# Optimization experiments

Measured on AMD Instinct MI355X. Metric: run time of the kernel, lower is better.

## Reference

```python
import jax, jax.numpy as jnp
import numpy as np

DIM, HEADS, DHEAD, CTX_DIM = 1024, 16, 64, 768
INNER = HEADS * DHEAD  # 1024
FF_HID = 4 * DIM       # 4096
EPS = 1e-5


def _ln(x, g, b):
    mu = jnp.mean(x, axis=-1, keepdims=True)
    var = jnp.mean(jnp.square(x - mu), axis=-1, keepdims=True)
    return (x - mu) * jax.lax.rsqrt(var + EPS) * g + b


def _attn(x, ctx, Wq, Wk, Wv, Wo, bo):
    b, n, _ = x.shape
    m = ctx.shape[1]
    q = (x @ Wq).reshape(b, n, HEADS, DHEAD)
    k = (ctx @ Wk).reshape(b, m, HEADS, DHEAD)
    v = (ctx @ Wv).reshape(b, m, HEADS, DHEAD)
    scale = DHEAD ** -0.5
    sim = jnp.einsum('bihd,bjhd->bhij', q, k) * scale
    attn = jax.nn.softmax(sim, axis=-1)
    out = jnp.einsum('bhij,bjhd->bihd', attn, v).reshape(b, n, INNER)
    return out @ Wo + bo


def setup_inputs() -> dict:
    key = jax.random.key(0)
    ks = jax.random.split(key, 24)
    def w(k, shape, fan_in):
        return jax.random.normal(k, shape, jnp.float32) * (fan_in ** -0.5)
    inp = {
        'x': jax.random.normal(ks[0], (2, 2048, DIM), jnp.float32),
        'context': jax.random.normal(ks[1], (2, 77, CTX_DIM), jnp.float32),
        # attn1 (self)
        'Wq1': w(ks[2], (DIM, INNER), DIM), 'Wk1': w(ks[3], (DIM, INNER), DIM),
        'Wv1': w(ks[4], (DIM, INNER), DIM), 'Wo1': w(ks[5], (INNER, DIM), INNER),
        'bo1': jnp.zeros((DIM,), jnp.float32),
        # attn2 (cross)
        'Wq2': w(ks[6], (DIM, INNER), DIM), 'Wk2': w(ks[7], (CTX_DIM, INNER), CTX_DIM),
        'Wv2': w(ks[8], (CTX_DIM, INNER), CTX_DIM), 'Wo2': w(ks[9], (INNER, DIM), INNER),
        'bo2': jnp.zeros((DIM,), jnp.float32),
        # GEGLU FFN
        'Wp': w(ks[10], (DIM, 2 * FF_HID), DIM), 'bp': jnp.zeros((2 * FF_HID,), jnp.float32),
        'W2': w(ks[11], (FF_HID, DIM), FF_HID), 'b2': jnp.zeros((DIM,), jnp.float32),
        # LayerNorms
        'g1': jnp.ones((DIM,), jnp.float32), 'be1': jnp.zeros((DIM,), jnp.float32),
        'g2': jnp.ones((DIM,), jnp.float32), 'be2': jnp.zeros((DIM,), jnp.float32),
        'g3': jnp.ones((DIM,), jnp.float32), 'be3': jnp.zeros((DIM,), jnp.float32),
    }
    return inp


def reference(x, context, Wq1, Wk1, Wv1, Wo1, bo1, Wq2, Wk2, Wv2, Wo2, bo2,
              Wp, bp, W2, b2, g1, be1, g2, be2, g3, be3):
    h = _ln(x, g1, be1)
    x = _attn(h, h, Wq1, Wk1, Wv1, Wo1, bo1) + x
    h = _ln(x, g2, be2)
    x = _attn(h, context, Wq2, Wk2, Wv2, Wo2, bo2) + x
    h = _ln(x, g3, be3)
    y = h @ Wp + bp
    a, gate = y[..., :FF_HID], y[..., FF_HID:]
    x = (a * jax.nn.gelu(gate, approximate=False)) @ W2 + b2 + x
    return x
```

## Files before the change

kernel.cpp:

```cpp
#include <hip/hip_runtime.h>
#include <hip/hip_bf16.h>
#include <math.h>

#define DIMN   1024
#define HEADS  16
#define DHEAD  64
#define CTXD   768
#define FFH    4096
#define NTOK   4096
#define SEQ    2048
#define NCTX   77
#define CTOK   154

typedef unsigned short u16;
typedef __bf16 bf16x8 __attribute__((ext_vector_type(8)));
typedef float  f32x4  __attribute__((ext_vector_type(4)));

__device__ __forceinline__ u16 f2bf(float f) {
  union { float f; unsigned u; } c; c.f = f;
  unsigned r = c.u + 0x7FFFu + ((c.u >> 16) & 1u);
  return (u16)(r >> 16);
}
__device__ __forceinline__ float bf2f(u16 h) {
  union { unsigned u; float f; } c; c.u = ((unsigned)h) << 16; return c.f;
}

__device__ __forceinline__ void gload16(const void* g, void* l) {
  __builtin_amdgcn_global_load_lds(
      (__attribute__((address_space(1))) void*)(void*)(g),
      (__attribute__((address_space(3))) void*)(l), 16, 0, 0);
}

__device__ __forceinline__ f32x4 mfma16(bf16x8 a, bf16x8 b, f32x4 c) {
  return __builtin_amdgcn_mfma_f32_16x16x32_bf16(a, b, c, 0, 0, 0);
}

struct WAll {
  int nw;
  int start[10];
  const float* s[10];
  u16* d[10];
  int K[10];
  int N[10];
};

__global__ __launch_bounds__(256)
void wconvA_k(WAll wa)
{
  __shared__ u16 t[64][65];
  const int bid = blockIdx.x;
  int w = 0;
  while (w + 1 < wa.nw && bid >= wa.start[w + 1]) ++w;
  const int local = bid - wa.start[w];
  const float* __restrict__ W  = wa.s[w];
  u16* __restrict__       WT   = wa.d[w];
  const int K = wa.K[w], N = wa.N[w];
  const int tilesX = N >> 6;
  const int n0 = (local % tilesX) * 64;
  const int k0 = (local / tilesX) * 64;
  const int tid = threadIdx.x;
  const int rr = tid >> 4, cc = tid & 15;
#pragma unroll
  for (int i = 0; i < 4; ++i) {
    int kr = rr + i * 16;
    const float4 v = *(const float4*)&W[(size_t)(k0 + kr) * N + n0 + cc * 4];
    t[kr][cc*4+0] = f2bf(v.x); t[kr][cc*4+1] = f2bf(v.y);
    t[kr][cc*4+2] = f2bf(v.z); t[kr][cc*4+3] = f2bf(v.w);
  }
  __syncthreads();
#pragma unroll
  for (int i = 0; i < 4; ++i) {
    int nr = rr + i * 16;
    int r0 = cc * 4;
    ushort4 o;
    o.x = t[r0+0][nr]; o.y = t[r0+1][nr]; o.z = t[r0+2][nr]; o.w = t[r0+3][nr];
    *(ushort4*)&WT[(size_t)(n0 + nr) * K + k0 + r0] = o;
  }
}

__global__ void cconv_k(const float* __restrict__ c, u16* __restrict__ o, int n)
{
  int i = blockIdx.x * 256 + threadIdx.x;
  if (i < n) o[i] = f2bf(c[i]);
}

__global__ __launch_bounds__(256)
void ln_k(const float* __restrict__ x, const float* __restrict__ gm,
          const float* __restrict__ bt, u16* __restrict__ o)
{
  int row = blockIdx.x;
  int tid = threadIdx.x;
  const float4 v = *(const float4*)&x[(size_t)row * DIMN + tid * 4];
  float s = v.x + v.y + v.z + v.w;
  float q = v.x*v.x + v.y*v.y + v.z*v.z + v.w*v.w;
#pragma unroll
  for (int off = 32; off; off >>= 1) { s += __shfl_xor(s, off); q += __shfl_xor(q, off); }
  __shared__ float ss[4], qq[4];
  int wave = tid >> 6;
  if ((tid & 63) == 0) { ss[wave] = s; qq[wave] = q; }
  __syncthreads();
  s = ss[0] + ss[1] + ss[2] + ss[3];
  q = qq[0] + qq[1] + qq[2] + qq[3];
  float mu = s * (1.0f / DIMN);
  float var = q * (1.0f / DIMN) - mu * mu;
  float rs = rsqrtf(var + 1e-5f);
  const float4 gv = *(const float4*)&gm[tid * 4];
  const float4 bv = *(const float4*)&bt[tid * 4];
  ushort4 r;
  r.x = f2bf((v.x - mu) * rs * gv.x + bv.x);
  r.y = f2bf((v.y - mu) * rs * gv.y + bv.y);
  r.z = f2bf((v.z - mu) * rs * gv.z + bv.z);
  r.w = f2bf((v.w - mu) * rs * gv.w + bv.w);
  *(ushort4*)&o[(size_t)row * DIMN + tid * 4] = r;
}

__global__ __launch_bounds__(256)
void ln_b_k(const u16* __restrict__ x, const float* __restrict__ gm,
            const float* __restrict__ bt, u16* __restrict__ o)
{
  int row = blockIdx.x;
  int tid = threadIdx.x;
  const ushort4 u = *(const ushort4*)&x[(size_t)row * DIMN + tid * 4];
  float4 v;
  v.x = bf2f(u.x); v.y = bf2f(u.y); v.z = bf2f(u.z); v.w = bf2f(u.w);
  float s = v.x + v.y + v.z + v.w;
  float q = v.x*v.x + v.y*v.y + v.z*v.z + v.w*v.w;
#pragma unroll
  for (int off = 32; off; off >>= 1) { s += __shfl_xor(s, off); q += __shfl_xor(q, off); }
  __shared__ float ss[4], qq[4];
  int wave = tid >> 6;
  if ((tid & 63) == 0) { ss[wave] = s; qq[wave] = q; }
  __syncthreads();
  s = ss[0] + ss[1] + ss[2] + ss[3];
  q = qq[0] + qq[1] + qq[2] + qq[3];
  float mu = s * (1.0f / DIMN);
  float var = q * (1.0f / DIMN) - mu * mu;
  float rs = rsqrtf(var + 1e-5f);
  const float4 gv = *(const float4*)&gm[tid * 4];
  const float4 bv = *(const float4*)&bt[tid * 4];
  ushort4 r;
  r.x = f2bf((v.x - mu) * rs * gv.x + bv.x);
  r.y = f2bf((v.y - mu) * rs * gv.y + bv.y);
  r.z = f2bf((v.z - mu) * rs * gv.z + bv.z);
  r.w = f2bf((v.w - mu) * rs * gv.w + bv.w);
  *(ushort4*)&o[(size_t)row * DIMN + tid * 4] = r;
}

template<int MODE>
__global__ __launch_bounds__(512, 4)
void gemm_k(const u16* __restrict__ A, const u16* __restrict__ Bt,
            int M, int N, int K,
            const float* __restrict__ bias, const float* __restrict__ resid,
            u16* __restrict__ obf, float* __restrict__ of32,
            int seq, int vstride,
            u16* __restrict__ ob2, u16* __restrict__ ob3)
{
  __shared__ __align__(16) u16 As[2][128 * 32];
  __shared__ __align__(16) u16 Bs[2][128 * 32];
  const int tid = threadIdx.x;
  const int lane = tid & 63, wave = tid >> 6;
  const int wr = wave >> 1, wc = wave & 1;
  const int g = lane >> 4, r16 = lane & 15;
  const int m0 = blockIdx.x * 128, n0 = blockIdx.y * 128;

  f32x4 acc[2][4] = {};

  const int srow = tid >> 2;
  const int sch  = tid & 3;
  const int schs = sch ^ ((srow >> 1) & 3);
  const int arow = (m0 + srow > M - 1) ? (M - 1) : (m0 + srow);
  const size_t abase = (size_t)arow * K + schs * 8;
  const size_t bbase = (size_t)(n0 + srow) * K + schs * 8;

  auto stage = [&](int buf, int kt) {
    gload16(A  + abase + kt, &As[buf][tid * 8]);
    gload16(Bt + bbase + kt, &Bs[buf][tid * 8]);
  };

  stage(0, 0);

  const int nkt = K >> 5;
  for (int t = 0; t < nkt; ++t) {
    const int cur = t & 1;
    if (t + 1 < nkt) {
      stage(cur ^ 1, (t + 1) << 5);
      asm volatile("s_waitcnt vmcnt(2)" ::: "memory");
    } else {
      asm volatile("s_waitcnt vmcnt(0)" ::: "memory");
    }
    __builtin_amdgcn_s_barrier();

    bf16x8 af[2], bfr[4];
#pragma unroll
    for (int mi = 0; mi < 2; ++mi) {
      int r = wr * 32 + mi * 16 + r16;
      int cph = g ^ ((r >> 1) & 3);
      af[mi] = *(const bf16x8*)&As[cur][(r * 4 + cph) * 8];
    }
#pragma unroll
    for (int ni = 0; ni < 4; ++ni) {
      int r = wc * 64 + ni * 16 + r16;
      int cph = g ^ ((r >> 1) & 3);
      bfr[ni] = *(const bf16x8*)&Bs[cur][(r * 4 + cph) * 8];
    }
    __builtin_amdgcn_s_setprio(1);
#pragma unroll
    for (int mi = 0; mi < 2; ++mi)
#pragma unroll
      for (int ni = 0; ni < 4; ++ni)
        acc[mi][ni] = mfma16(af[mi], bfr[ni], acc[mi][ni]);
    __builtin_amdgcn_s_setprio(0);

    __builtin_amdgcn_s_barrier();
  }

  const int grp = n0 >> 10;
#pragma unroll
  for (int ni = 0; ni < 4; ++ni) {
    int col = n0 + wc * 64 + ni * 16 + r16;
    const int c1 = col & 1023;
#pragma unroll
    for (int mi = 0; mi < 2; ++mi) {
      f32x4 c = acc[mi][ni];
#pragma unroll
      for (int rg = 0; rg < 4; ++rg) {
        int row = m0 + wr * 32 + mi * 16 + g * 4 + rg;
        if (row < M) {
          float v = c[rg];
          if constexpr (MODE == 4) {
            if (grp == 0) {
              obf[(size_t)row * 1024 + c1] = f2bf(v);
            } else if (grp == 1) {
              ob2[(size_t)row * 1024 + c1] = f2bf(v);
            } else {
              int b = row / seq, srow_ = row - b * seq;
              int jg = srow_ >> 6, j = srow_ & 63;
              int pos = jg * 64 + ((j & 15) << 2) + (j >> 4);
              ob3[((size_t)b * HEADS * DHEAD + c1) * vstride + pos] = f2bf(v);
            }
          }
        }
      }
    }
  }
  (void)bias; (void)resid; (void)of32;
}

template<int MODE>
__global__ __launch_bounds__(512, 2)
void gemm64_k(const u16* __restrict__ A, const u16* __restrict__ Bt,
              int M, int N, int K,
              const float* __restrict__ bias, const float* __restrict__ residf,
              const u16* __restrict__ residb,
              u16* __restrict__ obf, float* __restrict__ of32)
{
  __shared__ __align__(16) u16 As[2][128 * 64];
  __shared__ __align__(16) u16 Bs[2][128 * 64];
  const int tid = threadIdx.x;
  const int lane = tid & 63, wave = tid >> 6;
  const int wr = wave >> 1, wc = wave & 1;
  const int g = lane >> 4, r16 = lane & 15;
  const int m0 = blockIdx.x * 128, n0 = blockIdx.y * 128;

  f32x4 acc[2][4] = {};

  int aro[2], bro[2], scs[2];
#pragma unroll
  for (int i = 0; i < 2; ++i) {
    const int c = tid + i * 512;
    const int r = c >> 3, ch = c & 7;
    scs[i] = ch ^ (r & 7);
    aro[i] = (m0 + r > M - 1) ? (M - 1) : (m0 + r);
    bro[i] = n0 + r;
  }

  auto stage = [&](int buf, int kt) {
#pragma unroll
    for (int i = 0; i < 2; ++i) {
      const int c = tid + i * 512;
      gload16(A  + (size_t)aro[i] * K + kt + scs[i] * 8, &As[buf][c * 8]);
      gload16(Bt + (size_t)bro[i] * K + kt + scs[i] * 8, &Bs[buf][c * 8]);
    }
  };

  stage(0, 0);

  const int nkt = K >> 6;
  for (int t = 0; t < nkt; ++t) {
    const int cur = t & 1;
    if (t + 1 < nkt) {
      stage(cur ^ 1, (t + 1) << 6);
      asm volatile("s_waitcnt vmcnt(4)" ::: "memory");
    } else {
      asm volatile("s_waitcnt vmcnt(0)" ::: "memory");
    }
    __builtin_amdgcn_s_barrier();

#pragma unroll
    for (int ks = 0; ks < 2; ++ks) {
      bf16x8 af[2], bfr[4];
#pragma unroll
      for (int mi = 0; mi < 2; ++mi) {
        int r = wr * 32 + mi * 16 + r16;
        int cph = (ks * 4 + g) ^ (r & 7);
        af[mi] = *(const bf16x8*)&As[cur][(r * 8 + cph) * 8];
      }
#pragma unroll
      for (int ni = 0; ni < 4; ++ni) {
        int r = wc * 64 + ni * 16 + r16;
        int cph = (ks * 4 + g) ^ (r & 7);
        bfr[ni] = *(const bf16x8*)&Bs[cur][(r * 8 + cph) * 8];
      }
      __builtin_amdgcn_s_setprio(1);
#pragma unroll
      for (int mi = 0; mi < 2; ++mi)
#pragma unroll
        for (int ni = 0; ni < 4; ++ni)
          acc[mi][ni] = mfma16(af[mi], bfr[ni], acc[mi][ni]);
      __builtin_amdgcn_s_setprio(0);
    }

    __builtin_amdgcn_s_barrier();
  }

#pragma unroll
  for (int ni = 0; ni < 4; ++ni) {
    int col = n0 + wc * 64 + ni * 16 + r16;
    float bv = bias ? bias[col] : 0.0f;
#pragma unroll
    for (int mi = 0; mi < 2; ++mi) {
      f32x4 c = acc[mi][ni];
#pragma unroll
      for (int rg = 0; rg < 4; ++rg) {
        int row = m0 + wr * 32 + mi * 16 + g * 4 + rg;
        if (row < M) {
          float v = c[rg] + bv;
          size_t o = (size_t)row * N + col;
          if constexpr (MODE == 0) {
            obf[o] = f2bf(v);
          } else if constexpr (MODE == 6) {
            obf[o] = f2bf(v + residf[o]);
          } else if constexpr (MODE == 7) {
            obf[o] = f2bf(v + bf2f(residb[o]));
          } else {
            of32[o] = v + bf2f(residb[o]);
          }
        }
      }
    }
  }
}

__global__ __launch_bounds__(512, 2)
void q2kv2_k(const u16* __restrict__ hb, const u16* __restrict__ WqT2,
             u16* __restrict__ qb,
             const u16* __restrict__ ctxb, const u16* __restrict__ WkT2,
             u16* __restrict__ k2b, u16* __restrict__ vt2b)
{
  __shared__ __align__(16) u16 AsB[2][128 * 64];
  __shared__ __align__(16) u16 BsB[2][128 * 64];
  const int tid = threadIdx.x;
  const int lane = tid & 63, wave = tid >> 6;
  const int wr = wave >> 1, wc = wave & 1;
  const int g = lane >> 4, r16 = lane & 15;
  const int bid = blockIdx.x;

  if (bid < 256) {
    const int K = 1024;
    const int m0 = (bid & 31) * 128, n0 = (bid >> 5) * 128;
    f32x4 acc[2][4] = {};

    int aro[2], bro[2], scs[2];
#pragma unroll
    for (int i = 0; i < 2; ++i) {
      const int c = tid + i * 512;
      const int r = c >> 3, ch = c & 7;
      scs[i] = ch ^ (r & 7);
      aro[i] = m0 + r;
      bro[i] = n0 + r;
    }
    auto stage = [&](int buf, int kt) {
#pragma unroll
      for (int i = 0; i < 2; ++i) {
        const int c = tid + i * 512;
        gload16(hb   + (size_t)aro[i] * K + kt + scs[i] * 8, &AsB[buf][c * 8]);
        gload16(WqT2 + (size_t)bro[i] * K + kt + scs[i] * 8, &BsB[buf][c * 8]);
      }
    };
    stage(0, 0);
    const int nkt = K >> 6;
    for (int t = 0; t < nkt; ++t) {
      const int cur = t & 1;
      if (t + 1 < nkt) {
        stage(cur ^ 1, (t + 1) << 6);
        asm volatile("s_waitcnt vmcnt(4)" ::: "memory");
      } else {
        asm volatile("s_waitcnt vmcnt(0)" ::: "memory");
      }
      __builtin_amdgcn_s_barrier();
#pragma unroll
      for (int ks = 0; ks < 2; ++ks) {
        bf16x8 af[2], bfr[4];
#pragma unroll
        for (int mi = 0; mi < 2; ++mi) {
          int r = wr * 32 + mi * 16 + r16;
          int cph = (ks * 4 + g) ^ (r & 7);
          af[mi] = *(const bf16x8*)&AsB[cur][(r * 8 + cph) * 8];
        }
#pragma unroll
        for (int ni = 0; ni < 4; ++ni) {
          int r = wc * 64 + ni * 16 + r16;
          int cph = (ks * 4 + g) ^ (r & 7);
          bfr[ni] = *(const bf16x8*)&BsB[cur][(r * 8 + cph) * 8];
        }
        __builtin_amdgcn_s_setprio(1);
#pragma unroll
        for (int mi = 0; mi < 2; ++mi)
#pragma unroll
          for (int ni = 0; ni < 4; ++ni)
            acc[mi][ni] = mfma16(af[mi], bfr[ni], acc[mi][ni]);
        __builtin_amdgcn_s_setprio(0);
      }
      __builtin_amdgcn_s_barrier();
    }
#pragma unroll
    for (int ni = 0; ni < 4; ++ni) {
      int col = n0 + wc * 64 + ni * 16 + r16;
#pragma unroll
      for (int mi = 0; mi < 2; ++mi) {
#pragma unroll
        for (int rg = 0; rg < 4; ++rg) {
          int row = m0 + wr * 32 + mi * 16 + g * 4 + rg;
          qb[(size_t)row * 1024 + col] = f2bf(acc[mi][ni][rg]);
        }
      }
    }
  } else {
    const int K = 768, M = CTOK;
    const int local = bid - 256;
    const int m0 = (local & 1) * 128, n0 = (local >> 1) * 128;
    u16* As = &AsB[0][0];
    u16* Bs = &BsB[0][0];
    const int BUFS = 128 * 32;
    f32x4 acc[2][4] = {};

    const int srow = tid >> 2;
    const int sch  = tid & 3;
    const int schs = sch ^ ((srow >> 1) & 3);
    const int arow = (m0 + srow > M - 1) ? (M - 1) : (m0 + srow);
    const size_t abase = (size_t)arow * K + schs * 8;
    const size_t bbase = (size_t)(n0 + srow) * K + schs * 8;

    auto stage = [&](int buf, int kt) {
      gload16(ctxb + abase + kt, &As[buf * BUFS + tid * 8]);
      gload16(WkT2 + bbase + kt, &Bs[buf * BUFS + tid * 8]);
    };
    stage(0, 0);
    const int nkt = K >> 5;
    for (int t = 0; t < nkt; ++t) {
      const int cur = t & 1;
      if (t + 1 < nkt) {
        stage(cur ^ 1, (t + 1) << 5);
        asm volatile("s_waitcnt vmcnt(2)" ::: "memory");
      } else {
        asm volatile("s_waitcnt vmcnt(0)" ::: "memory");
      }
      __builtin_amdgcn_s_barrier();

      bf16x8 af[2], bfr[4];
#pragma unroll
      for (int mi = 0; mi < 2; ++mi) {
        int r = wr * 32 + mi * 16 + r16;
        int cph = g ^ ((r >> 1) & 3);
        af[mi] = *(const bf16x8*)&As[cur * BUFS + (r * 4 + cph) * 8];
      }
#pragma unroll
      for (int ni = 0; ni < 4; ++ni) {
        int r = wc * 64 + ni * 16 + r16;
        int cph = g ^ ((r >> 1) & 3);
        bfr[ni] = *(const bf16x8*)&Bs[cur * BUFS + (r * 4 + cph) * 8];
      }
      __builtin_amdgcn_s_setprio(1);
#pragma unroll
      for (int mi = 0; mi < 2; ++mi)
#pragma unroll
        for (int ni = 0; ni < 4; ++ni)
          acc[mi][ni] = mfma16(af[mi], bfr[ni], acc[mi][ni]);
      __builtin_amdgcn_s_setprio(0);

      __builtin_amdgcn_s_barrier();
    }

    const int grp = n0 >> 10;
#pragma unroll
    for (int ni = 0; ni < 4; ++ni) {
      int col = n0 + wc * 64 + ni * 16 + r16;
      const int c1 = col & 1023;
#pragma unroll
      for (int mi = 0; mi < 2; ++mi) {
#pragma unroll
        for (int rg = 0; rg < 4; ++rg) {
          int row = m0 + wr * 32 + mi * 16 + g * 4 + rg;
          if (row < M) {
            float v = acc[mi][ni][rg];
            if (grp == 0) {
              k2b[(size_t)row * 1024 + c1] = f2bf(v);
            } else {
              int b = row / NCTX, srow_ = row - b * NCTX;
              int jg = srow_ >> 6, j = srow_ & 63;
              int pos = jg * 64 + ((j & 15) << 2) + (j >> 4);
              vt2b[((size_t)b * HEADS * DHEAD + c1) * 128 + pos] = f2bf(v);
            }
          }
        }
      }
    }
  }
}

__global__ __launch_bounds__(512, 2)
void geglu_k(const u16* __restrict__ A, const u16* __restrict__ B1t,
             const u16* __restrict__ B2t,
             const float* __restrict__ ba, const float* __restrict__ bg,
             u16* __restrict__ out, int M, int N)
{
  __shared__ __align__(16) u16 As[2][128 * 32];
  __shared__ __align__(16) u16 B1s[2][128 * 32];
  __shared__ __align__(16) u16 B2s[2][128 * 32];
  const int tid = threadIdx.x;
  const int lane = tid & 63, wave = tid >> 6;
  const int wr = wave >> 1, wc = wave & 1;
  const int g = lane >> 4, r16 = lane & 15;
  const int m0 = blockIdx.x * 128, n0 = blockIdx.y * 128;
  const int K = 1024;

  f32x4 acca[2][4] = {}, accg[2][4] = {};

  const int srow = tid >> 2;
  const int sch  = tid & 3;
  const int schs = sch ^ ((srow >> 1) & 3);
  const size_t abase = (size_t)(m0 + srow) * K + schs * 8;
  const size_t bbase = (size_t)(n0 + srow) * K + schs * 8;

  auto stage = [&](int buf, int kt) {
    gload16(A   + abase + kt, &As[buf][tid * 8]);
    gload16(B1t + bbase + kt, &B1s[buf][tid * 8]);
    gload16(B2t + bbase + kt, &B2s[buf][tid * 8]);
  };

  stage(0, 0);

  const int nkt = K >> 5;
  for (int t = 0; t < nkt; ++t) {
    const int cur = t & 1;
    if (t + 1 < nkt) {
      stage(cur ^ 1, (t + 1) << 5);
      asm volatile("s_waitcnt vmcnt(3)" ::: "memory");
    } else {
      asm volatile("s_waitcnt vmcnt(0)" ::: "memory");
    }
    __builtin_amdgcn_s_barrier();

    bf16x8 af[2], b1f[4], b2f[4];
#pragma unroll
    for (int mi = 0; mi < 2; ++mi) {
      int r = wr * 32 + mi * 16 + r16;
      int cph = g ^ ((r >> 1) & 3);
      af[mi] = *(const bf16x8*)&As[cur][(r * 4 + cph) * 8];
    }
#pragma unroll
    for (int ni = 0; ni < 4; ++ni) {
      int r = wc * 64 + ni * 16 + r16;
      int cph = g ^ ((r >> 1) & 3);
      b1f[ni] = *(const bf16x8*)&B1s[cur][(r * 4 + cph) * 8];
      b2f[ni] = *(const bf16x8*)&B2s[cur][(r * 4 + cph) * 8];
    }
    __builtin_amdgcn_s_setprio(1);
#pragma unroll
    for (int mi = 0; mi < 2; ++mi)
#pragma unroll
      for (int ni = 0; ni < 4; ++ni) {
        acca[mi][ni] = mfma16(af[mi], b1f[ni], acca[mi][ni]);
        accg[mi][ni] = mfma16(af[mi], b2f[ni], accg[mi][ni]);
      }
    __builtin_amdgcn_s_setprio(0);

    __builtin_amdgcn_s_barrier();
  }

#pragma unroll
  for (int ni = 0; ni < 4; ++ni) {
    int col = n0 + wc * 64 + ni * 16 + r16;
    float bva = ba[col], bvg = bg[col];
#pragma unroll
    for (int mi = 0; mi < 2; ++mi) {
#pragma unroll
      for (int rg = 0; rg < 4; ++rg) {
        int row = m0 + wr * 32 + mi * 16 + g * 4 + rg;
        float a  = acca[mi][ni][rg] + bva;
        float gt = accg[mi][ni][rg] + bvg;
        float gl = 0.5f * gt * (1.0f + erff(gt * 0.70710678f));
        out[(size_t)row * N + col] = f2bf(a * gl);
      }
    }
  }
}

__global__ __launch_bounds__(512, 1)
void attn_k(const u16* __restrict__ q, const u16* __restrict__ k,
            const u16* __restrict__ vt, u16* __restrict__ o,
            int kvlen, int seqk, int vstride)
{
  __shared__ __align__(16) u16 Ks[2][128 * 64];
  __shared__ __align__(16) u16 Vs[2][64 * 128];
  __shared__ __align__(16) u16 Ps[8][32 * 136];
  const int tid = threadIdx.x, lane = tid & 63, wave = tid >> 6;
  const int g = lane >> 4, r16 = lane & 15;

  const int L  = blockIdx.y * 8 + blockIdx.x;
  const int c8 = L & 7, tt = L >> 3;
  const int bx = tt & 7;
  const int bh = c8 * 4 + (tt >> 3);

  const int b = bh >> 4, h = bh & 15;
  const int q0 = bx * 256 + wave * 32;
  const float C = 0.18033688f;

  bf16x8 aq[2][2];
#pragma unroll
  for (int qs = 0; qs < 2; ++qs) {
    const size_t qoff = (size_t)(b * SEQ + q0 + qs * 16 + r16) * DIMN + h * DHEAD;
#pragma unroll
    for (int kc = 0; kc < 2; ++kc)
      aq[qs][kc] = *(const bf16x8*)&q[qoff + kc * 32 + g * 8];
  }
  asm volatile("" :: "v"(aq[0][0]), "v"(aq[0][1]), "v"(aq[1][0]), "v"(aq[1][1]));

  f32x4 oacc[2][4] = {};
  float mi[2][4], li[2][4];
#pragma unroll
  for (int qs = 0; qs < 2; ++qs)
#pragma unroll
    for (int rg = 0; rg < 4; ++rg) { mi[qs][rg] = -3e38f; li[qs][rg] = 0.f; }

  const size_t vtbase = (size_t)(b * HEADS + h) * DHEAD * vstride;
  const size_t kbase  = (size_t)b * seqk * DIMN + h * DHEAD;
  const int nkv = (kvlen + 127) >> 7;

  auto stage = [&](int buf, int kv0) {
#pragma unroll
    for (int i = 0; i < 2; ++i) {
      const int c = tid + i * 512;
      const int row = c >> 3, ch = c & 7;
      const int chs = ch ^ (row & 7);
      int kr = kv0 + row; if (kr > kvlen - 1) kr = kvlen - 1;
      gload16(k + kbase + (size_t)kr * DIMN + chs * 8, &Ks[buf][c * 8]);
    }
#pragma unroll
    for (int i = 0; i < 2; ++i) {
      const int c = tid + i * 512;
      const int row = c >> 4, ch = c & 15;
      const int chs = ch ^ (row & 15);
      gload16(vt + vtbase + (size_t)row * vstride + kv0 + chs * 8, &Vs[buf][c * 8]);
    }
  };

  stage(0, 0);

  for (int kvb = 0; kvb < nkv; ++kvb) {
    const int kv0 = kvb * 128;
    const int cur = kvb & 1;
    if (kvb + 1 < nkv) {
      stage(cur ^ 1, kv0 + 128);
      asm volatile("s_waitcnt vmcnt(4)" ::: "memory");
    } else {
      asm volatile("s_waitcnt vmcnt(0)" ::: "memory");
    }
    __builtin_amdgcn_s_barrier();

    f32x4 sa[2][8];
#pragma unroll
    for (int qs = 0; qs < 2; ++qs)
#pragma unroll
      for (int st = 0; st < 8; ++st) sa[qs][st] = (f32x4){0.f, 0.f, 0.f, 0.f};
    __builtin_amdgcn_s_setprio(1);
#pragma unroll
    for (int st = 0; st < 8; ++st) {
      const int kvr = st * 16 + r16;
#pragma unroll
      for (int kc = 0; kc < 2; ++kc) {
        const int chs = (kc * 4 + g) ^ (kvr & 7);
        const bf16x8 kf = *(const bf16x8*)&Ks[cur][kvr * 64 + chs * 8];
        sa[0][st] = mfma16(aq[0][kc], kf, sa[0][st]);
        sa[1][st] = mfma16(aq[1][kc], kf, sa[1][st]);
      }
    }
    __builtin_amdgcn_s_setprio(0);

    if (kv0 + 128 > kvlen) {
#pragma unroll
      for (int st = 0; st < 8; ++st)
        if (kv0 + st * 16 + r16 >= kvlen) {
#pragma unroll
          for (int qs = 0; qs < 2; ++qs)
#pragma unroll
            for (int rg = 0; rg < 4; ++rg) sa[qs][st][rg] = -3e38f;
        }
    }

    float bad = 0.f;
    float m4v[2][4];
#pragma unroll
    for (int qs = 0; qs < 2; ++qs)
#pragma unroll
      for (int rg = 0; rg < 4; ++rg) {
        float m4 = fmaxf(fmaxf(sa[qs][0][rg], sa[qs][1][rg]),
                         fmaxf(sa[qs][2][rg], sa[qs][3][rg]));
        m4 = fmaxf(m4, fmaxf(fmaxf(sa[qs][4][rg], sa[qs][5][rg]),
                             fmaxf(sa[qs][6][rg], sa[qs][7][rg])));
        m4v[qs][rg] = m4;
        bad = fmaxf(bad, m4 - mi[qs][rg]);
      }
    if (__any(bad > 16.0f)) {
#pragma unroll
      for (int qs = 0; qs < 2; ++qs)
#pragma unroll
        for (int rg = 0; rg < 4; ++rg) {
          float mx = m4v[qs][rg];
#pragma unroll
          for (int off = 1; off < 16; off <<= 1) mx = fmaxf(mx, __shfl_xor(mx, off));
          const float nm = fmaxf(mi[qs][rg], mx);
          const float corr = __builtin_amdgcn_exp2f((mi[qs][rg] - nm) * C);
          mi[qs][rg] = nm;
          li[qs][rg] *= corr;
#pragma unroll
          for (int ds = 0; ds < 4; ++ds) oacc[qs][ds][rg] *= corr;
        }
    }

#pragma unroll
    for (int qs = 0; qs < 2; ++qs) {
#pragma unroll
      for (int rg = 0; rg < 4; ++rg) {
        const float mc = mi[qs][rg] * C;
        float p[8];
#pragma unroll
        for (int st = 0; st < 8; ++st)
          p[st] = __builtin_amdgcn_exp2f(__builtin_fmaf(sa[qs][st][rg], C, -mc));
        li[qs][rg] += ((p[0] + p[1]) + (p[2] + p[3])) + ((p[4] + p[5]) + (p[6] + p[7]));
        unsigned w0, w1, w2, w3;
        asm("v_cvt_pk_bf16_f32 %0, %1, %2" : "=v"(w0) : "v"(p[0]), "v"(p[1]));
        asm("v_cvt_pk_bf16_f32 %0, %1, %2" : "=v"(w1) : "v"(p[2]), "v"(p[3]));
        asm("v_cvt_pk_bf16_f32 %0, %1, %2" : "=v"(w2) : "v"(p[4]), "v"(p[5]));
        asm("v_cvt_pk_bf16_f32 %0, %1, %2" : "=v"(w3) : "v"(p[6]), "v"(p[7]));
        const int prow = qs * 16 + g * 4 + rg;
        uint2 pk0; pk0.x = w0; pk0.y = w1;
        uint2 pk1; pk1.x = w2; pk1.y = w3;
        *(uint2*)&Ps[wave][prow * 136 + r16 * 4]      = pk0;
        *(uint2*)&Ps[wave][prow * 136 + 64 + r16 * 4] = pk1;
      }
    }

    __builtin_amdgcn_s_setprio(1);
#pragma unroll
    for (int kc = 0; kc < 4; ++kc) {
      const bf16x8 pa0 = *(const bf16x8*)&Ps[wave][(r16)      * 136 + kc * 32 + g * 8];
      const bf16x8 pa1 = *(const bf16x8*)&Ps[wave][(16 + r16) * 136 + kc * 32 + g * 8];
#pragma unroll
      for (int ds = 0; ds < 4; ++ds) {
        const int dr = ds * 16 + r16;
        const int cc = kc * 4 + g;
        const int chs = cc ^ (dr & 15);
        const bf16x8 vf = *(const bf16x8*)&Vs[cur][dr * 128 + chs * 8];
        oacc[0][ds] = mfma16(pa0, vf, oacc[0][ds]);
        oacc[1][ds] = mfma16(pa1, vf, oacc[1][ds]);
      }
    }
    __builtin_amdgcn_s_setprio(0);

    __builtin_amdgcn_s_barrier();
  }

#pragma unroll
  for (int qs = 0; qs < 2; ++qs)
#pragma unroll
    for (int rg = 0; rg < 4; ++rg) {
      float s = li[qs][rg];
#pragma unroll
      for (int off = 1; off < 16; off <<= 1) s += __shfl_xor(s, off);
      li[qs][rg] = s;
    }

#pragma unroll
  for (int qs = 0; qs < 2; ++qs)
#pragma unroll
    for (int rg = 0; rg < 4; ++rg) {
      const float inv = 1.0f / li[qs][rg];
      const int row = q0 + qs * 16 + g * 4 + rg;
      const size_t base = (size_t)(b * SEQ + row) * DIMN + h * DHEAD;
#pragma unroll
      for (int ds = 0; ds < 4; ++ds)
        o[base + ds * 16 + r16] = f2bf(oacc[qs][ds][rg] * inv);
    }
}

extern "C" void kernel_launch(void* const* d_in, const int* in_sizes, int n_in,
                              void* d_out, int out_size, void* d_ws, size_t ws_size,
                              hipStream_t stream)
{
  const float* x   = (const float*)d_in[0];
  const float* ctx = (const float*)d_in[1];
  const float* Wq1 = (const float*)d_in[2];
  const float* Wk1 = (const float*)d_in[3];
  const float* Wv1 = (const float*)d_in[4];
  const float* Wo1 = (const float*)d_in[5];
  const float* bo1 = (const float*)d_in[6];
  const float* Wq2 = (const float*)d_in[7];
  const float* Wk2 = (const float*)d_in[8];
  const float* Wv2 = (const float*)d_in[9];
  const float* Wo2 = (const float*)d_in[10];
  const float* bo2 = (const float*)d_in[11];
  const float* Wp  = (const float*)d_in[12];
  const float* bp  = (const float*)d_in[13];
  const float* W2  = (const float*)d_in[14];
  const float* b2  = (const float*)d_in[15];
  const float* g1  = (const float*)d_in[16];
  const float* be1 = (const float*)d_in[17];
  const float* g2  = (const float*)d_in[18];
  const float* be2 = (const float*)d_in[19];
  const float* g3  = (const float*)d_in[20];
  const float* be3 = (const float*)d_in[21];

  char* ws = (char*)d_ws;
  size_t off = 0;
  auto alloc = [&](size_t bytes) -> void* {
    void* p = ws + off;
    off += (bytes + 255) & ~(size_t)255;
    return p;
  };

  u16* WqT1 = (u16*)alloc((size_t)1024 * 1024 * 2);
  u16* WkT1 = (u16*)alloc((size_t)1024 * 1024 * 2);
  u16* WvT1 = (u16*)alloc((size_t)1024 * 1024 * 2);
  u16* WoT1 = (u16*)alloc((size_t)1024 * 1024 * 2);
  u16* WqT2 = (u16*)alloc((size_t)1024 * 1024 * 2);
  u16* WkT2 = (u16*)alloc((size_t)1024 * 768 * 2);
  u16* WvT2 = (u16*)alloc((size_t)1024 * 768 * 2);
  u16* WoT2 = (u16*)alloc((size_t)1024 * 1024 * 2);
  u16* WpT  = (u16*)alloc((size_t)8192 * 1024 * 2);
  u16* W2T  = (u16*)alloc((size_t)1024 * 4096 * 2);
  u16* x1b  = (u16*)alloc((size_t)NTOK * DIMN * 2);
  u16* x2b  = (u16*)alloc((size_t)NTOK * DIMN * 2);
  u16* ctxb = (u16*)alloc((size_t)CTOK * CTXD * 2);
  u16* k2b  = (u16*)alloc((size_t)CTOK * DIMN * 2);
  u16* vt2b = (u16*)alloc((size_t)2 * HEADS * DHEAD * 128 * 2);
  u16* hb   = (u16*)alloc((size_t)NTOK * DIMN * 2);
  u16* qb   = (u16*)alloc((size_t)NTOK * DIMN * 2);
  u16* kb   = (u16*)alloc((size_t)NTOK * DIMN * 2);
  u16* vtb  = (u16*)alloc((size_t)NTOK * DIMN * 2);
  u16* ab   = (u16*)alloc((size_t)NTOK * DIMN * 2);
  u16* ub   = qb;

  dim3 blk(256);
  dim3 blk5(512);

  WAll wa;
  wa.nw = 10;
  const float* srcs[10] = {Wq1, Wk1, Wv1, Wo1, Wq2, Wo2, Wk2, Wv2, Wp, W2};
  u16* dsts[10]         = {WqT1, WkT1, WvT1, WoT1, WqT2, WoT2, WkT2, WvT2, WpT, W2T};
  const int Ksz[10]     = {1024, 1024, 1024, 1024, 1024, 1024, 768, 768, 1024, 4096};
  const int Nsz[10]     = {1024, 1024, 1024, 1024, 1024, 1024, 1024, 1024, 8192, 1024};
  int tot = 0;
  for (int i = 0; i < 10; ++i) {
    wa.start[i] = tot; wa.s[i] = srcs[i]; wa.d[i] = dsts[i];
    wa.K[i] = Ksz[i];  wa.N[i] = Nsz[i];
    tot += (Nsz[i] >> 6) * (Ksz[i] >> 6);
  }
  wconvA_k<<<dim3(tot), blk, 0, stream>>>(wa);
  cconv_k<<<dim3((CTOK * CTXD + 255) / 256), blk, 0, stream>>>(ctx, ctxb, CTOK * CTXD);

  ln_k<<<NTOK, 256, 0, stream>>>(x, g1, be1, hb);
  gemm_k<4><<<dim3(32, 24), blk5, 0, stream>>>(hb, WqT1, NTOK, 3072, 1024, nullptr, nullptr, qb, nullptr, SEQ, SEQ, kb, vtb);
  attn_k<<<dim3(8, 32), blk5, 0, stream>>>(qb, kb, vtb, ab, SEQ, SEQ, SEQ);
  gemm64_k<6><<<dim3(32, 8), blk5, 0, stream>>>(ab, WoT1, NTOK, 1024, 1024, bo1, x, nullptr, x1b, nullptr);

  ln_b_k<<<NTOK, 256, 0, stream>>>(x1b, g2, be2, hb);
  q2kv2_k<<<dim3(288), blk5, 0, stream>>>(hb, WqT2, qb, ctxb, WkT2, k2b, vt2b);
  attn_k<<<dim3(8, 32), blk5, 0, stream>>>(qb, k2b, vt2b, ab, NCTX, NCTX, 128);
  gemm64_k<7><<<dim3(32, 8), blk5, 0, stream>>>(ab, WoT2, NTOK, 1024, 1024, bo2, nullptr, x1b, x2b, nullptr);

  ln_b_k<<<NTOK, 256, 0, stream>>>(x2b, g3, be3, hb);
  geglu_k<<<dim3(32, 32), blk5, 0, stream>>>(hb, WpT, WpT + (size_t)4096 * 1024, bp, bp + 4096, ub, NTOK, FFH);
  gemm64_k<8><<<dim3(32, 8), blk5, 0, stream>>>(ub, W2T, NTOK, 1024, 4096, b2, nullptr, x2b, nullptr, (float*)d_out);

  (void)in_sizes; (void)n_in; (void)out_size; (void)ws_size;
}
```

Before: 369.9 us.

## Fold LN1 and context conversion into weight-convert launch; widen QKV GEMM K-tile

Merges the context bf16 conversion and the first LayerNorm into the weight-transpose kernel as extra block ranges, removing two kernel launches. Replaces the K=32-step QKV projection GEMM with a dedicated K=64-step version that uses larger LDS tiles and an 8-way swizzle, halving the barrier and loop iterations. The larger shared memory footprint lowers occupancy (launch bounds drop from 4 to 2 blocks per CU). Block-range dispatch adds some branching to the convert kernel.

Result: no change. 364.3 us (-1.5%).

```diff
diff --git a/kernel.cpp b/kernel.cpp
--- a/kernel.cpp
+++ b/kernel.cpp
@@ -42,13 +42,50 @@
   u16* d[10];
   int K[10];
   int N[10];
+  int lnStart, ccStart;
+  const float* x; const float* g1; const float* be1; u16* hb;
+  const float* ctx; u16* ctxb;
 };
 
 __global__ __launch_bounds__(256)
 void wconvA_k(WAll wa)
 {
   __shared__ u16 t[64][65];
+  __shared__ float ss[4], qq[4];
   const int bid = blockIdx.x;
+  const int tid = threadIdx.x;
+
+  if (bid >= wa.ccStart) {
+    const int i = (bid - wa.ccStart) * 256 + tid;
+    if (i < CTOK * CTXD) wa.ctxb[i] = f2bf(wa.ctx[i]);
+    return;
+  }
+  if (bid >= wa.lnStart) {
+    const int row = bid - wa.lnStart;
+    const float4 v = *(const float4*)&wa.x[(size_t)row * DIMN + tid * 4];
+    float s = v.x + v.y + v.z + v.w;
+    float q = v.x*v.x + v.y*v.y + v.z*v.z + v.w*v.w;
+#pragma unroll
+    for (int off = 32; off; off >>= 1) { s += __shfl_xor(s, off); q += __shfl_xor(q, off); }
+    const int wave = tid >> 6;
+    if ((tid & 63) == 0) { ss[wave] = s; qq[wave] = q; }
+    __syncthreads();
+    s = ss[0] + ss[1] + ss[2] + ss[3];
+    q = qq[0] + qq[1] + qq[2] + qq[3];
+    const float mu = s * (1.0f / DIMN);
+    const float var = q * (1.0f / DIMN) - mu * mu;
+    const float rs = rsqrtf(var + 1e-5f);
+    const float4 gv = *(const float4*)&wa.g1[tid * 4];
+    const float4 bv = *(const float4*)&wa.be1[tid * 4];
+    ushort4 r;
+    r.x = f2bf((v.x - mu) * rs * gv.x + bv.x);
+    r.y = f2bf((v.y - mu) * rs * gv.y + bv.y);
+    r.z = f2bf((v.z - mu) * rs * gv.z + bv.z);
+    r.w = f2bf((v.w - mu) * rs * gv.w + bv.w);
+    *(ushort4*)&wa.hb[(size_t)row * DIMN + tid * 4] = r;
+    return;
+  }
+
   int w = 0;
   while (w + 1 < wa.nw && bid >= wa.start[w + 1]) ++w;
   const int local = bid - wa.start[w];
@@ -58,7 +95,6 @@
   const int tilesX = N >> 6;
   const int n0 = (local % tilesX) * 64;
   const int k0 = (local / tilesX) * 64;
-  const int tid = threadIdx.x;
   const int rr = tid >> 4, cc = tid & 15;
 #pragma unroll
   for (int i = 0; i < 4; ++i) {
@@ -78,19 +114,15 @@
   }
 }
 
-__global__ void cconv_k(const float* __restrict__ c, u16* __restrict__ o, int n)
-{
-  int i = blockIdx.x * 256 + threadIdx.x;
-  if (i < n) o[i] = f2bf(c[i]);
-}
-
 __global__ __launch_bounds__(256)
-void ln_k(const float* __restrict__ x, const float* __restrict__ gm,
-          const float* __restrict__ bt, u16* __restrict__ o)
+void ln_b_k(const u16* __restrict__ x, const float* __restrict__ gm,
+            const float* __restrict__ bt, u16* __restrict__ o)
 {
   int row = blockIdx.x;
   int tid = threadIdx.x;
-  const float4 v = *(const float4*)&x[(size_t)row * DIMN + tid * 4];
+  const ushort4 u = *(const ushort4*)&x[(size_t)row * DIMN + tid * 4];
+  float4 v;
+  v.x = bf2f(u.x); v.y = bf2f(u.y); v.z = bf2f(u.z); v.w = bf2f(u.w);
   float s = v.x + v.y + v.z + v.w;
   float q = v.x*v.x + v.y*v.y + v.z*v.z + v.w*v.w;
 #pragma unroll
@@ -114,102 +146,76 @@
   *(ushort4*)&o[(size_t)row * DIMN + tid * 4] = r;
 }
 
-__global__ __launch_bounds__(256)
-void ln_b_k(const u16* __restrict__ x, const float* __restrict__ gm,
-            const float* __restrict__ bt, u16* __restrict__ o)
+__global__ __launch_bounds__(512, 2)
+void qkv64_k(const u16* __restrict__ A, const u16* __restrict__ Bt,
+             u16* __restrict__ qb, u16* __restrict__ kb, u16* __restrict__ vtb)
 {
-  int row = blockIdx.x;
-  int tid = threadIdx.x;
-  const ushort4 u = *(const ushort4*)&x[(size_t)row * DIMN + tid * 4];
-  float4 v;
-  v.x = bf2f(u.x); v.y = bf2f(u.y); v.z = bf2f(u.z); v.w = bf2f(u.w);
-  float s = v.x + v.y + v.z + v.w;
-  float q = v.x*v.x + v.y*v.y + v.z*v.z + v.w*v.w;
-#pragma unroll
-  for (int off = 32; off; off >>= 1) { s += __shfl_xor(s, off); q += __shfl_xor(q, off); }
-  __shared__ float ss[4], qq[4];
-  int wave = tid >> 6;
-  if ((tid & 63) == 0) { ss[wave] = s; qq[wave] = q; }
-  __syncthreads();
-  s = ss[0] + ss[1] + ss[2] + ss[3];
-  q = qq[0] + qq[1] + qq[2] + qq[3];
-  float mu = s * (1.0f / DIMN);
-  float var = q * (1.0f / DIMN) - mu * mu;
-  float rs = rsqrtf(var + 1e-5f);
-  const float4 gv = *(const float4*)&gm[tid * 4];
-  const float4 bv = *(const float4*)&bt[tid * 4];
-  ushort4 r;
-  r.x = f2bf((v.x - mu) * rs * gv.x + bv.x);
-  r.y = f2bf((v.y - mu) * rs * gv.y + bv.y);
-  r.z = f2bf((v.z - mu) * rs * gv.z + bv.z);
-  r.w = f2bf((v.w - mu) * rs * gv.w + bv.w);
-  *(ushort4*)&o[(size_t)row * DIMN + tid * 4] = r;
-}
-
-template<int MODE>
-__global__ __launch_bounds__(512, 4)
-void gemm_k(const u16* __restrict__ A, const u16* __restrict__ Bt,
-            int M, int N, int K,
-            const float* __restrict__ bias, const float* __restrict__ resid,
-            u16* __restrict__ obf, float* __restrict__ of32,
-            int seq, int vstride,
-            u16* __restrict__ ob2, u16* __restrict__ ob3)
-{
-  __shared__ __align__(16) u16 As[2][128 * 32];
-  __shared__ __align__(16) u16 Bs[2][128 * 32];
+  __shared__ __align__(16) u16 As[2][128 * 64];
+  __shared__ __align__(16) u16 Bs[2][128 * 64];
   const int tid = threadIdx.x;
   const int lane = tid & 63, wave = tid >> 6;
   const int wr = wave >> 1, wc = wave & 1;
   const int g = lane >> 4, r16 = lane & 15;
   const int m0 = blockIdx.x * 128, n0 = blockIdx.y * 128;
+  const int K = 1024;
 
   f32x4 acc[2][4] = {};
 
-  const int srow = tid >> 2;
-  const int sch  = tid & 3;
-  const int schs = sch ^ ((srow >> 1) & 3);
-  const int arow = (m0 + srow > M - 1) ? (M - 1) : (m0 + srow);
-  const size_t abase = (size_t)arow * K + schs * 8;
-  const size_t bbase = (size_t)(n0 + srow) * K + schs * 8;
+  int aro[2], bro[2], scs[2];
+#pragma unroll
+  for (int i = 0; i < 2; ++i) {
+    const int c = tid + i * 512;
+    const int r = c >> 3, ch = c & 7;
+    scs[i] = ch ^ (r & 7);
+    aro[i] = m0 + r;
+    bro[i] = n0 + r;
+  }
 
   auto stage = [&](int buf, int kt) {
-    gload16(A  + abase + kt, &As[buf][tid * 8]);
-    gload16(Bt + bbase + kt, &Bs[buf][tid * 8]);
+#pragma unroll
+    for (int i = 0; i < 2; ++i) {
+      const int c = tid + i * 512;
+      gload16(A  + (size_t)aro[i] * K + kt + scs[i] * 8, &As[buf][c * 8]);
+      gload16(Bt + (size_t)bro[i] * K + kt + scs[i] * 8, &Bs[buf][c * 8]);
+    }
   };
 
   stage(0, 0);
 
-  const int nkt = K >> 5;
+  const int nkt = K >> 6;
   for (int t = 0; t < nkt; ++t) {
     const int cur = t & 1;
     if (t + 1 < nkt) {
-      stage(cur ^ 1, (t + 1) << 5);
-      asm volatile("s_waitcnt vmcnt(2)" ::: "memory");
+      stage(cur ^ 1, (t + 1) << 6);
+      asm volatile("s_waitcnt vmcnt(4)" ::: "memory");
     } else {
       asm volatile("s_waitcnt vmcnt(0)" ::: "memory");
     }
     __builtin_amdgcn_s_barrier();
 
-    bf16x8 af[2], bfr[4];
-#pragma unroll
-    for (int mi = 0; mi < 2; ++mi) {
-      int r = wr * 32 + mi * 16 + r16;
-      int cph = g ^ ((r >> 1) & 3);
-      af[mi] = *(const bf16x8*)&As[cur][(r * 4 + cph) * 8];
-    }
-#pragma unroll
-    for (int ni = 0; ni < 4; ++ni) {
-      int r = wc * 64 + ni * 16 + r16;
-      int cph = g ^ ((r >> 1) & 3);
-      bfr[ni] = *(const bf16x8*)&Bs[cur][(r * 4 + cph) * 8];
-    }
-    __builtin_amdgcn_s_setprio(1);
-#pragma unroll
-    for (int mi = 0; mi < 2; ++mi)
-#pragma unroll
-      for (int ni = 0; ni < 4; ++ni)
-        acc[mi][ni] = mfma16(af[mi], bfr[ni], acc[mi][ni]);
-    __builtin_amdgcn_s_setprio(0);
+#pragma unroll
+    for (int ks = 0; ks < 2; ++ks) {
+      bf16x8 af[2], bfr[4];
+#pragma unroll
+      for (int mi = 0; mi < 2; ++mi) {
+        int r = wr * 32 + mi * 16 + r16;
+        int cph = (ks * 4 + g) ^ (r & 7);
+        af[mi] = *(const bf16x8*)&As[cur][(r * 8 + cph) * 8];
+      }
+#pragma unroll
+      for (int ni = 0; ni < 4; ++ni) {
+        int r = wc * 64 + ni * 16 + r16;
+        int cph = (ks * 4 + g) ^ (r & 7);
+        bfr[ni] = *(const bf16x8*)&Bs[cur][(r * 8 + cph) * 8];
+      }
+      __builtin_amdgcn_s_setprio(1);
+#pragma unroll
+      for (int mi = 0; mi < 2; ++mi)
+#pragma unroll
+        for (int ni = 0; ni < 4; ++ni)
+          acc[mi][ni] = mfma16(af[mi], bfr[ni], acc[mi][ni]);
+      __builtin_amdgcn_s_setprio(0);
+    }
 
     __builtin_amdgcn_s_barrier();
   }
@@ -221,29 +227,23 @@
     const int c1 = col & 1023;
 #pragma unroll
     for (int mi = 0; mi < 2; ++mi) {
-      f32x4 c = acc[mi][ni];
 #pragma unroll
       for (int rg = 0; rg < 4; ++rg) {
         int row = m0 + wr * 32 + mi * 16 + g * 4 + rg;
-        if (row < M) {
-          float v = c[rg];
-          if constexpr (MODE == 4) {
-            if (grp == 0) {
-              obf[(size_t)row * 1024 + c1] = f2bf(v);
-            } else if (grp == 1) {
-              ob2[(size_t)row * 1024 + c1] = f2bf(v);
-            } else {
-              int b = row / seq, srow_ = row - b * seq;
-              int jg = srow_ >> 6, j = srow_ & 63;
-              int pos = jg * 64 + ((j & 15) << 2) + (j >> 4);
-              ob3[((size_t)b * HEADS * DHEAD + c1) * vstride + pos] = f2bf(v);
-            }
-          }
+        float v = acc[mi][ni][rg];
+        if (grp == 0) {
+          qb[(size_t)row * 1024 + c1] = f2bf(v);
+        } else if (grp == 1) {
+          kb[(size_t)row * 1024 + c1] = f2bf(v);
+        } else {
+          int b = row >> 11, srow_ = row & 2047;
+          int jg = srow_ >> 6, j = srow_ & 63;
+          int pos = jg * 64 + ((j & 15) << 2) + (j >> 4);
+          vtb[((size_t)b * HEADS * DHEAD + c1) * SEQ + pos] = f2bf(v);
         }
       }
     }
   }
-  (void)bias; (void)resid; (void)of32;
 }
 
 template<int MODE>
@@ -876,11 +876,14 @@
     wa.K[i] = Ksz[i];  wa.N[i] = Nsz[i];
     tot += (Nsz[i] >> 6) * (Ksz[i] >> 6);
   }
-  wconvA_k<<<dim3(tot), blk, 0, stream>>>(wa);
-  cconv_k<<<dim3((CTOK * CTXD + 255) / 256), blk, 0, stream>>>(ctx, ctxb, CTOK * CTXD);
-
-  ln_k<<<NTOK, 256, 0, stream>>>(x, g1, be1, hb);
-  gemm_k<4><<<dim3(32, 24), blk5, 0, stream>>>(hb, WqT1, NTOK, 3072, 1024, nullptr, nullptr, qb, nullptr, SEQ, SEQ, kb, vtb);
+  wa.lnStart = tot;
+  wa.ccStart = tot + NTOK;
+  wa.x = x; wa.g1 = g1; wa.be1 = be1; wa.hb = hb;
+  wa.ctx = ctx; wa.ctxb = ctxb;
+  const int ccBlocks = (CTOK * CTXD + 255) / 256;
+  wconvA_k<<<dim3(tot + NTOK + ccBlocks), blk, 0, stream>>>(wa);
+
+  qkv64_k<<<dim3(32, 24), blk5, 0, stream>>>(hb, WqT1, qb, kb, vtb);
   attn_k<<<dim3(8, 32), blk5, 0, stream>>>(qb, kb, vtb, ab, SEQ, SEQ, SEQ);
   gemm64_k<6><<<dim3(32, 8), blk5, 0, stream>>>(ab, WoT1, NTOK, 1024, 1024, bo1, x, nullptr, x1b, nullptr);
 
```
